# Optimization experiments

Hardware: AMD Instinct MI355X
Metric: run time of the kernel (lower is better)

The kernel has to match this reference:

```python
import jax, jax.numpy as jnp
import numpy as np

D_MODEL = 1024
NEG_BIG = -1e9  # matches TF float32 branch


def setup_inputs() -> dict:
    key = jax.random.key(0)
    kq, kk, kv, km = jax.random.split(key, 4)
    B, S, D = 4, 2048, D_MODEL
    q = jax.random.normal(kq, (B, S, D), dtype=jnp.float32)
    k = jax.random.normal(kk, (B, S, D), dtype=jnp.float32)
    v = jax.random.normal(kv, (B, S, D), dtype=jnp.float32)
    mask = jax.random.randint(km, (B, 1, S), 0, 2, dtype=jnp.int32)  # 1 = masked
    return {"q": q, "k": k, "v": v, "mask": mask}


def reference(q, k, v, mask):
    scale = jnp.asarray(D_MODEL, q.dtype) ** -0.5
    # [B,S,S] attention logits
    logits = jnp.einsum("bqd,bkd->bqk", q, k) * scale
    logits = logits + mask.astype(q.dtype) * NEG_BIG
    weights = jax.nn.softmax(logits, axis=-1)
    return jnp.einsum("bqk,bkd->bqd", weights, v)
```

## Files before the change

kernel.cpp:

```cpp
#include <hip/hip_runtime.h>
#include <hip/hip_bf16.h>
#include <cstdint>

#define B_    4
#define S_    2048
#define D_    1024
#define SCALE 0.03125f
#define NEG_BIG -1e9f

typedef __attribute__((ext_vector_type(8))) short short8;
typedef __attribute__((ext_vector_type(4))) float f32x4;

__device__ __forceinline__ ushort f2bf(float f) {
  uint32_t u = __float_as_uint(f);
  u += 0x7fffu + ((u >> 16) & 1u);
  return (ushort)(u >> 16);
}

__device__ __forceinline__ float bf2f(ushort h) {
  return __uint_as_float((uint32_t)h << 16);
}

__device__ __forceinline__ void load16_to_lds(const void* g, void* l) {
  __builtin_amdgcn_global_load_lds(
      (const __attribute__((address_space(1))) uint32_t*)g,
      (__attribute__((address_space(3))) uint32_t*)l, 16, 0, 0);
}

__global__ void prep(const float* __restrict__ Q, const float* __restrict__ K,
                     const float* __restrict__ V, ushort* __restrict__ Qb,
                     ushort* __restrict__ Kb, ushort* __restrict__ Vt) {
  __shared__ ushort tile[64][68];
  int id = blockIdx.x;
  if (id < 8192) {
    const float* X = (id < 4096) ? Q : K;
    ushort* Xb     = (id < 4096) ? Qb : Kb;
    int cid = id & 4095;
    size_t i = ((size_t)cid * 256 + threadIdx.x) * 8;
    float4 a = *(const float4*)(X + i);
    float4 c = *(const float4*)(X + i + 4);
    uint4 w;
    w.x = (uint)f2bf(a.x) | ((uint)f2bf(a.y) << 16);
    w.y = (uint)f2bf(a.z) | ((uint)f2bf(a.w) << 16);
    w.z = (uint)f2bf(c.x) | ((uint)f2bf(c.y) << 16);
    w.w = (uint)f2bf(c.z) | ((uint)f2bf(c.w) << 16);
    *(uint4*)(Xb + i) = w;
    return;
  }
  int t = id - 8192;
  int s0 = (t & 31) * 64, d0 = ((t >> 5) & 15) * 64, b = t >> 9;
  int tx = threadIdx.x & 15, ty = threadIdx.x >> 4;
  const float* src = V + ((size_t)b * S_ + s0) * D_ + d0;
  for (int i = 0; i < 4; ++i) {
    int row = ty + i * 16;
    float4 a = *(const float4*)(src + (size_t)row * D_ + tx * 4);
    ushort4 w;
    w.x = f2bf(a.x); w.y = f2bf(a.y); w.z = f2bf(a.z); w.w = f2bf(a.w);
    *(ushort4*)&tile[row][tx * 4] = w;
  }
  __syncthreads();
  ushort* dst = Vt + ((size_t)b * D_ + d0) * S_ + s0;
  for (int i = 0; i < 4; ++i) {
    int drow = ty + i * 16;
    ushort4 w;
    w.x = tile[tx * 4 + 0][drow];
    w.y = tile[tx * 4 + 1][drow];
    w.z = tile[tx * 4 + 2][drow];
    w.w = tile[tx * 4 + 3][drow];
    *(ushort4*)(dst + (size_t)drow * S_ + tx * 4) = w;
  }
}

template<int KDIM, int LDA, int LDB, int LDC,
         long long BATCHA, long long BATCHB, long long BATCHC, int EPI, typename OutT>
__global__ void gemm_bt(const ushort* __restrict__ A, const ushort* __restrict__ Bt,
                        OutT* __restrict__ C, const int* __restrict__ mask) {
  __shared__ __align__(16) ushort As[128 * 32];
  __shared__ __align__(16) ushort Bs[128 * 32];

  int linear = blockIdx.x;
  int xcd = linear & 7, idx = linear >> 3;
  int b = xcd >> 1, half = xcd & 1;
  int bm, bn;
  if (EPI == 0) {
    bm = idx >> 3;
    int s = idx & 7;
    bn = half * 8 + ((bm & 1) ? 7 - s : s);
  } else {
    int bmh = idx >> 3;
    bm = half * 8 + bmh;
    int s = idx & 7;
    bn = (bmh & 1) ? 7 - s : s;
  }

  int tid  = threadIdx.x;
  int lane = tid & 63;
  int wave = tid >> 6;
  int l16 = lane & 15, quad = lane >> 4;
  int wm = (wave & 1) * 64, wn = (wave >> 1) * 64;

  float madd[4];
  if (EPI == 0) {
#pragma unroll
    for (int nt = 0; nt < 4; ++nt)
      madd[nt] = mask[b * S_ + bn * 128 + wn + nt * 16 + l16] ? NEG_BIG : 0.f;
  }

  const ushort* Ab = A  + (size_t)b * BATCHA + (size_t)(bm * 128) * LDA;
  const ushort* Bb = Bt + (size_t)b * BATCHB + (size_t)(bn * 128) * LDB;

  f32x4 acc[4][4];
#pragma unroll
  for (int i = 0; i < 4; ++i)
#pragma unroll
    for (int j = 0; j < 4; ++j) acc[i][j] = (f32x4){0.f, 0.f, 0.f, 0.f};

  for (int kc = 0; kc < KDIM / 32; ++kc) {
    __syncthreads();
#pragma unroll
    for (int h = 0; h < 2; ++h) {
      int c = tid + h * 256;
      const ushort* ga = Ab + (size_t)(c >> 2) * LDA + kc * 32 + (c & 3) * 8;
      const ushort* gb = Bb + (size_t)(c >> 2) * LDB + kc * 32 + (c & 3) * 8;
      load16_to_lds(ga, As + c * 8);
      load16_to_lds(gb, Bs + c * 8);
    }
    __syncthreads();

    short8 af[4], bf[4];
#pragma unroll
    for (int mt = 0; mt < 4; ++mt)
      af[mt] = *(const short8*)(As + (wm + mt * 16 + l16) * 32 + quad * 8);
#pragma unroll
    for (int nt = 0; nt < 4; ++nt)
      bf[nt] = *(const short8*)(Bs + (wn + nt * 16 + l16) * 32 + quad * 8);
#pragma unroll
    for (int mt = 0; mt < 4; ++mt)
#pragma unroll
      for (int nt = 0; nt < 4; ++nt)
        acc[mt][nt] = __builtin_amdgcn_mfma_f32_16x16x32_bf16(af[mt], bf[nt], acc[mt][nt], 0, 0, 0);
  }

  OutT* Cb = C + (size_t)b * BATCHC + (size_t)(bm * 128) * LDC + bn * 128;
#pragma unroll
  for (int nt = 0; nt < 4; ++nt) {
    int col = wn + nt * 16 + l16;
#pragma unroll
    for (int mt = 0; mt < 4; ++mt)
#pragma unroll
      for (int r = 0; r < 4; ++r) {
        int row = wm + mt * 16 + quad * 4 + r;
        float v = acc[mt][nt][r];
        if (EPI == 0)
          Cb[(size_t)row * LDC + col] = (OutT)f2bf(v * SCALE + madd[nt]);
        else
          Cb[(size_t)row * LDC + col] = (OutT)v;
      }
  }
}

__global__ void softmax_rows(const ushort* __restrict__ S, ushort* __restrict__ P) {
  int row = blockIdx.x * 4 + (threadIdx.x >> 6);
  int lane = threadIdx.x & 63;
  const ushort* src = S + (size_t)row * S_;

  float x[32];
#pragma unroll
  for (int j = 0; j < 4; ++j) {
    uint4 v = *(const uint4*)(src + lane * 8 + j * 512);
    uint32_t w[4] = {v.x, v.y, v.z, v.w};
#pragma unroll
    for (int t = 0; t < 4; ++t) {
      x[j * 8 + t * 2 + 0] = __uint_as_float(w[t] << 16);
      x[j * 8 + t * 2 + 1] = __uint_as_float(w[t] & 0xffff0000u);
    }
  }
  float m = x[0];
#pragma unroll
  for (int i = 1; i < 32; ++i) m = fmaxf(m, x[i]);
  for (int off = 1; off < 64; off <<= 1) m = fmaxf(m, __shfl_xor(m, off));

  float e[32], s = 0.f;
#pragma unroll
  for (int i = 0; i < 32; ++i) { e[i] = __expf(x[i] - m); s += e[i]; }
  for (int off = 1; off < 64; off <<= 1) s += __shfl_xor(s, off);
  float rinv = 1.0f / s;

  ushort* dst = P + (size_t)row * S_;
#pragma unroll
  for (int j = 0; j < 4; ++j) {
    uint4 w;
    uint32_t* pw = &w.x;
#pragma unroll
    for (int t = 0; t < 4; ++t)
      pw[t] = (uint32_t)f2bf(e[j * 8 + t * 2] * rinv) |
              ((uint32_t)f2bf(e[j * 8 + t * 2 + 1] * rinv) << 16);
    *(uint4*)(dst + lane * 8 + j * 512) = w;
  }
}

extern "C" void kernel_launch(void* const* d_in, const int* in_sizes, int n_in,
                              void* d_out, int out_size, void* d_ws, size_t ws_size,
                              hipStream_t stream) {
  const float* Q   = (const float*)d_in[0];
  const float* K   = (const float*)d_in[1];
  const float* V   = (const float*)d_in[2];
  const int*  mask = (const int*)d_in[3];
  float* Out = (float*)d_out;

  const size_t E = (size_t)B_ * S_ * D_;
  ushort* Qb = (ushort*)d_ws;
  ushort* Kb = Qb + E;
  ushort* Vt = Kb + E;
  ushort* Sb = Vt + E;
  ushort* P  = Qb;

  prep<<<10240, 256, 0, stream>>>(Q, K, V, Qb, Kb, Vt);

  gemm_bt<1024, 1024, 1024, 2048,
          (long long)2048 * 1024, (long long)2048 * 1024, (long long)2048 * 2048, 0, ushort>
      <<<1024, 256, 0, stream>>>(Qb, Kb, Sb, mask);

  softmax_rows<<<2048, 256, 0, stream>>>(Sb, P);

  gemm_bt<2048, 2048, 2048, 1024,
          (long long)2048 * 2048, (long long)1024 * 2048, (long long)2048 * 1024, 1, float>
      <<<512, 256, 0, stream>>>(P, Vt, Out, nullptr);
}
```

Before: 237.0 us.

## Rewrite GEMMs with 256x128 tiles, triple-buffered LDS pipeline and XOR swizzle

Measured after the change: 229.6 us. 1.03x faster.

```diff
diff --git a/kernel.cpp b/kernel.cpp
--- a/kernel.cpp
+++ b/kernel.cpp
@@ -1,5 +1,4 @@
 #include <hip/hip_runtime.h>
-#include <hip/hip_bf16.h>
 #include <cstdint>
 
 #define B_    4
@@ -15,10 +14,6 @@
   uint32_t u = __float_as_uint(f);
   u += 0x7fffu + ((u >> 16) & 1u);
   return (ushort)(u >> 16);
-}
-
-__device__ __forceinline__ float bf2f(ushort h) {
-  return __uint_as_float((uint32_t)h << 16);
 }
 
 __device__ __forceinline__ void load16_to_lds(const void* g, void* l) {
@@ -72,42 +67,40 @@
 }
 
 template<int KDIM, int LDA, int LDB, int LDC,
-         long long BATCHA, long long BATCHB, long long BATCHC, int EPI, typename OutT>
-__global__ void gemm_bt(const ushort* __restrict__ A, const ushort* __restrict__ Bt,
-                        OutT* __restrict__ C, const int* __restrict__ mask) {
-  __shared__ __align__(16) ushort As[128 * 32];
-  __shared__ __align__(16) ushort Bs[128 * 32];
-
-  int linear = blockIdx.x;
-  int xcd = linear & 7, idx = linear >> 3;
-  int b = xcd >> 1, half = xcd & 1;
-  int bm, bn;
-  if (EPI == 0) {
-    bm = idx >> 3;
-    int s = idx & 7;
-    bn = half * 8 + ((bm & 1) ? 7 - s : s);
-  } else {
-    int bmh = idx >> 3;
-    bm = half * 8 + bmh;
-    int s = idx & 7;
-    bn = (bmh & 1) ? 7 - s : s;
-  }
+         long long BATCHA, long long BATCHB, long long BATCHC,
+         int NBN, int EPI, typename OutT>
+__global__ __launch_bounds__(512, 2)
+void gemm2(const ushort* __restrict__ A, const ushort* __restrict__ Bt,
+           OutT* __restrict__ C, const int* __restrict__ mask) {
+  constexpr int SLOT = (256 + 128) * 64;
+  constexpr int BOFF = 256 * 64;
+  constexpr int NT   = KDIM / 64;
+  __shared__ __align__(16) ushort lds[3 * SLOT];
+
+  const int per = gridDim.x >> 3;
+  int g = (blockIdx.x & 7) * per + (blockIdx.x >> 3);
+  constexpr int TPB = 8 * NBN;
+  int b  = g / TPB;
+  int t0 = g % TPB;
+  int bm = t0 / NBN;
+  int sn = t0 % NBN;
+  int bn = (bm & 1) ? (NBN - 1 - sn) : sn;
 
   int tid  = threadIdx.x;
   int lane = tid & 63;
   int wave = tid >> 6;
+  int wr = wave >> 1, wc = wave & 1;
   int l16 = lane & 15, quad = lane >> 4;
-  int wm = (wave & 1) * 64, wn = (wave >> 1) * 64;
+
+  const ushort* Ab = A  + (size_t)b * BATCHA + (size_t)(bm * 256) * LDA;
+  const ushort* Bb = Bt + (size_t)b * BATCHB + (size_t)(bn * 128) * LDB;
 
   float madd[4];
   if (EPI == 0) {
 #pragma unroll
     for (int nt = 0; nt < 4; ++nt)
-      madd[nt] = mask[b * S_ + bn * 128 + wn + nt * 16 + l16] ? NEG_BIG : 0.f;
-  }
-
-  const ushort* Ab = A  + (size_t)b * BATCHA + (size_t)(bm * 128) * LDA;
-  const ushort* Bb = Bt + (size_t)b * BATCHB + (size_t)(bn * 128) * LDB;
+      madd[nt] = mask[b * S_ + bn * 128 + wc * 64 + nt * 16 + l16] ? NEG_BIG : 0.f;
+  }
 
   f32x4 acc[4][4];
 #pragma unroll
@@ -115,41 +108,108 @@
 #pragma unroll
     for (int j = 0; j < 4; ++j) acc[i][j] = (f32x4){0.f, 0.f, 0.f, 0.f};
 
-  for (int kc = 0; kc < KDIM / 32; ++kc) {
-    __syncthreads();
-#pragma unroll
-    for (int h = 0; h < 2; ++h) {
-      int c = tid + h * 256;
-      const ushort* ga = Ab + (size_t)(c >> 2) * LDA + kc * 32 + (c & 3) * 8;
-      const ushort* gb = Bb + (size_t)(c >> 2) * LDB + kc * 32 + (c & 3) * 8;
-      load16_to_lds(ga, As + c * 8);
-      load16_to_lds(gb, Bs + c * 8);
-    }
-    __syncthreads();
-
-    short8 af[4], bf[4];
+  auto stage = [&](int kt, int slot) {
+#pragma unroll
+    for (int j = 0; j < 4; ++j) {
+      int c = tid + j * 512;
+      int row  = c >> 3;
+      int col8 = (c & 7) * 8;
+      int src8 = col8 ^ ((row & 7) << 3);
+      load16_to_lds(Ab + (size_t)row * LDA + (size_t)kt * 64 + src8,
+                    lds + slot * SLOT + c * 8);
+    }
+#pragma unroll
+    for (int j = 0; j < 2; ++j) {
+      int c = tid + j * 512;
+      int row  = c >> 3;
+      int col8 = (c & 7) * 8;
+      int src8 = col8 ^ ((row & 7) << 3);
+      load16_to_lds(Bb + (size_t)row * LDB + (size_t)kt * 64 + src8,
+                    lds + slot * SLOT + BOFF + c * 8);
+    }
+  };
+
+  stage(0, 0);
+  stage(1, 1);
+  asm volatile("s_waitcnt vmcnt(6)\n"
+               "s_barrier" ::: "memory");
+
+  int sc = 0;
+  for (int t = 0; t < NT; ++t) {
+    int s2 = sc + 2; if (s2 >= 3) s2 -= 3;
+    if (t + 2 < NT) stage(t + 2, s2);
+
+    const ushort* La = lds + sc * SLOT;
+    const ushort* Lb = lds + sc * SLOT + BOFF;
+
+    short8 a0[2][2], bfr[4][2];
+#pragma unroll
+    for (int ks = 0; ks < 2; ++ks) {
+#pragma unroll
+      for (int mt = 0; mt < 2; ++mt) {
+        int row  = wr * 64 + mt * 16 + l16;
+        int col8 = (ks * 32 + quad * 8) ^ ((row & 7) << 3);
+        a0[mt][ks] = *(const short8*)(La + row * 64 + col8);
+      }
+#pragma unroll
+      for (int nt = 0; nt < 4; ++nt) {
+        int row  = wc * 64 + nt * 16 + l16;
+        int col8 = (ks * 32 + quad * 8) ^ ((row & 7) << 3);
+        bfr[nt][ks] = *(const short8*)(Lb + row * 64 + col8);
+      }
+    }
+    __builtin_amdgcn_s_setprio(1);
+#pragma unroll
+    for (int ks = 0; ks < 2; ++ks)
+#pragma unroll
+      for (int mt = 0; mt < 2; ++mt)
+#pragma unroll
+        for (int nt = 0; nt < 4; ++nt)
+          acc[mt][nt] = __builtin_amdgcn_mfma_f32_16x16x32_bf16(
+              a0[mt][ks], bfr[nt][ks], acc[mt][nt], 0, 0, 0);
+    __builtin_amdgcn_s_setprio(0);
+    asm volatile("s_barrier" ::: "memory");
+
+    short8 a1[2][2];
+#pragma unroll
+    for (int ks = 0; ks < 2; ++ks)
+#pragma unroll
+      for (int mt = 0; mt < 2; ++mt) {
+        int row  = wr * 64 + (mt + 2) * 16 + l16;
+        int col8 = (ks * 32 + quad * 8) ^ ((row & 7) << 3);
+        a1[mt][ks] = *(const short8*)(La + row * 64 + col8);
+      }
+    __builtin_amdgcn_s_setprio(1);
+#pragma unroll
+    for (int ks = 0; ks < 2; ++ks)
+#pragma unroll
+      for (int mt = 0; mt < 2; ++mt)
+#pragma unroll
+        for (int nt = 0; nt < 4; ++nt)
+          acc[mt + 2][nt] = __builtin_amdgcn_mfma_f32_16x16x32_bf16(
+              a1[mt][ks], bfr[nt][ks], acc[mt + 2][nt], 0, 0, 0);
+    __builtin_amdgcn_s_setprio(0);
+
+    if (t < NT - 3)
+      asm volatile("s_waitcnt lgkmcnt(0)\n"
+                   "s_waitcnt vmcnt(6)\n"
+                   "s_barrier" ::: "memory");
+    else
+      asm volatile("s_waitcnt lgkmcnt(0)\n"
+                   "s_waitcnt vmcnt(0)\n"
+                   "s_barrier" ::: "memory");
+    sc = (sc == 2) ? 0 : sc + 1;
+  }
+
+  OutT* Cb = C + (size_t)b * BATCHC + (size_t)(bm * 256) * LDC + (size_t)(bn * 128);
+#pragma unroll
+  for (int nt = 0; nt < 4; ++nt) {
+    int col = wc * 64 + nt * 16 + l16;
 #pragma unroll
     for (int mt = 0; mt < 4; ++mt)
-      af[mt] = *(const short8*)(As + (wm + mt * 16 + l16) * 32 + quad * 8);
-#pragma unroll
-    for (int nt = 0; nt < 4; ++nt)
-      bf[nt] = *(const short8*)(Bs + (wn + nt * 16 + l16) * 32 + quad * 8);
-#pragma unroll
-    for (int mt = 0; mt < 4; ++mt)
-#pragma unroll
-      for (int nt = 0; nt < 4; ++nt)
-        acc[mt][nt] = __builtin_amdgcn_mfma_f32_16x16x32_bf16(af[mt], bf[nt], acc[mt][nt], 0, 0, 0);
-  }
-
-  OutT* Cb = C + (size_t)b * BATCHC + (size_t)(bm * 128) * LDC + bn * 128;
-#pragma unroll
-  for (int nt = 0; nt < 4; ++nt) {
-    int col = wn + nt * 16 + l16;
-#pragma unroll
-    for (int mt = 0; mt < 4; ++mt)
 #pragma unroll
       for (int r = 0; r < 4; ++r) {
-        int row = wm + mt * 16 + quad * 4 + r;
+        int row = wr * 64 + mt * 16 + quad * 4 + r;
         float v = acc[mt][nt][r];
         if (EPI == 0)
           Cb[(size_t)row * LDC + col] = (OutT)f2bf(v * SCALE + madd[nt]);
@@ -217,13 +277,15 @@
 
   prep<<<10240, 256, 0, stream>>>(Q, K, V, Qb, Kb, Vt);
 
-  gemm_bt<1024, 1024, 1024, 2048,
-          (long long)2048 * 1024, (long long)2048 * 1024, (long long)2048 * 2048, 0, ushort>
-      <<<1024, 256, 0, stream>>>(Qb, Kb, Sb, mask);
+  gemm2<1024, 1024, 1024, 2048,
+        (long long)2048 * 1024, (long long)2048 * 1024, (long long)2048 * 2048,
+        16, 0, ushort>
+      <<<512, 512, 0, stream>>>(Qb, Kb, Sb, mask);
 
   softmax_rows<<<2048, 256, 0, stream>>>(Sb, P);
 
-  gemm_bt<2048, 2048, 2048, 1024,
-          (long long)2048 * 2048, (long long)1024 * 2048, (long long)2048 * 1024, 1, float>
-      <<<512, 256, 0, stream>>>(P, Vt, Out, nullptr);
-}
+  gemm2<2048, 2048, 2048, 1024,
+        (long long)2048 * 2048, (long long)1024 * 2048, (long long)2048 * 1024,
+        8, 1, float>
+      <<<256, 512, 0, stream>>>(P, Vt, Out, nullptr);
+}
```
